# Kernel tuning notes

Measured on AMD Instinct MI355X. Metric: run time of the kernel, lower is better.

The kernel has to match this reference:

```python
import jax, jax.numpy as jnp
import numpy as np

B, D, K = 2048, 512, 32  # pairs, input_dim, feature_map_dim


def setup_inputs() -> dict:
    key = jax.random.key(0)
    k1, k2, kw, kv, ku = jax.random.split(key, 5)
    x1 = jax.random.normal(k1, (B, D), dtype=jnp.float32)
    x2 = jax.random.normal(k2, (B, D), dtype=jnp.float32)
    # glorot-style scaled params
    W = jax.random.normal(kw, (D, D, K), dtype=jnp.float32) * (1.0 / np.sqrt(D))
    V = jax.random.normal(kv, (K, 2 * D), dtype=jnp.float32) * (1.0 / np.sqrt(2 * D))
    U = jax.random.normal(ku, (K, 1), dtype=jnp.float32)
    b = jnp.zeros((K,), dtype=jnp.float32)
    return {"x1": x1, "x2": x2, "W": W, "V": V, "U": U, "b": b}


def reference(x1, x2, W, V, U, b):
    # Bilinear term: h[b,k] = x1[b]^T W[:,:,k] x2[b]
    h = jnp.einsum('bd,dek,be->bk', x1, W, x2)
    # Linear term: V[k] . concat(x1, x2)   (loop's V_out, batched)
    v_out = jnp.concatenate([x1, x2], axis=1) @ V.T  # [B, K]
    scores = jax.nn.relu(h + v_out + b)              # inneract
    # output per pair: sum_k U[k] * scores[k]
    return scores @ U[:, 0]  # [B]
```

## Files before the change

### kernel.cpp

```cpp
#include <hip/hip_runtime.h>
#include <hip/hip_bf16.h>


#define BATCH 2048
#define DIM 512
#define KF 32
#define NCOL (DIM * KF)
#define JT (NCOL / 128)

typedef __attribute__((ext_vector_type(8))) short bf16x8;
typedef __attribute__((ext_vector_type(4))) float f32x4;
typedef __attribute__((address_space(1))) const unsigned int gas_u32;
typedef __attribute__((address_space(3))) unsigned int las_u32;

static __device__ __forceinline__ ushort f2bf(float x) {
    __hip_bfloat16 h = __float2bfloat16(x);
    union { __hip_bfloat16 h; ushort u; } cv; cv.h = h;
    return cv.u;
}

__global__ void fused_prep_kernel(const float* __restrict__ x1,
                                  const float* __restrict__ x2,
                                  const float* __restrict__ W,
                                  const float* __restrict__ V,
                                  ushort* __restrict__ x1b,
                                  ushort* __restrict__ Wt,
                                  float* __restrict__ vout) {
    __shared__ __align__(16) char sbuf[32768];
    const int bx = blockIdx.x;
    const int t = threadIdx.x;

    if (bx < 256) {
        float (*xs)[1024] = (float(*)[1024])sbuf;
        const int b0 = bx * 8;
        #pragma unroll
        for (int it = 0; it < 4; ++it) {
            int q = it * 256 + t;
            int r = q >> 7;
            int c = (q & 127) * 4;
            *(float4*)&xs[r][c]       = *(const float4*)&x1[(size_t)(b0 + r) * DIM + c];
            *(float4*)&xs[r][512 + c] = *(const float4*)&x2[(size_t)(b0 + r) * DIM + c];
        }
        __syncthreads();
        const int lane = t & 63, w = t >> 6;
        #pragma unroll
        for (int rr = 0; rr < 2; ++rr) {
            const int r = w * 2 + rr;
            float4 xv[4];
            #pragma unroll
            for (int i = 0; i < 4; ++i)
                xv[i] = *(const float4*)&xs[r][i * 256 + lane * 4];
            #pragma unroll
            for (int k0 = 0; k0 < KF; k0 += 4) {
                float s[4] = {0.f, 0.f, 0.f, 0.f};
                #pragma unroll
                for (int kk = 0; kk < 4; ++kk) {
                    const float* vrow = V + (size_t)(k0 + kk) * 1024;
                    #pragma unroll
                    for (int i = 0; i < 4; ++i) {
                        float4 vv = *(const float4*)&vrow[i * 256 + lane * 4];
                        s[kk] += vv.x * xv[i].x + vv.y * xv[i].y + vv.z * xv[i].z + vv.w * xv[i].w;
                    }
                }
                #pragma unroll
                for (int kk = 0; kk < 4; ++kk) {
                    float v = s[kk];
                    #pragma unroll
                    for (int off = 32; off; off >>= 1) v += __shfl_down(v, off);
                    if (lane == 0) vout[(size_t)(b0 + r) * KF + k0 + kk] = v;
                }
            }
        }
    } else if (bx < 1280) {
        int i = (bx - 256) * 256 + t;
        float4 v = *((const float4*)x1 + i);
        ushort4 r;
        r.x = f2bf(v.x); r.y = f2bf(v.y); r.z = f2bf(v.z); r.w = f2bf(v.w);
        *((ushort4*)x1b + i) = r;
    } else {
        ushort (*lt)[65] = (ushort(*)[65])sbuf;
        const int bxl = bx - 1280;
        const int n0 = (bxl >> 3) * 64;
        const int d0 = (bxl & 7) * 64;
        #pragma unroll
        for (int it = 0; it < 4; ++it) {
            int q = it * 256 + t;
            int dl = q >> 4;
            int n4 = (q & 15) * 4;
            float4 v = *(const float4*)&W[(size_t)(d0 + dl) * NCOL + n0 + n4];
            lt[n4 + 0][dl] = f2bf(v.x);
            lt[n4 + 1][dl] = f2bf(v.y);
            lt[n4 + 2][dl] = f2bf(v.z);
            lt[n4 + 3][dl] = f2bf(v.w);
        }
        __syncthreads();
        #pragma unroll
        for (int it = 0; it < 4; ++it) {
            int q = it * 256 + t;
            int nl = q >> 4;
            int d4 = (q & 15) * 4;
            ushort4 o;
            o.x = lt[nl][d4 + 0]; o.y = lt[nl][d4 + 1];
            o.z = lt[nl][d4 + 2]; o.w = lt[nl][d4 + 3];
            *(ushort4*)&Wt[(size_t)(n0 + nl) * DIM + d0 + d4] = o;
        }
    }
}

__global__ void gemm_fused_kernel(const ushort* __restrict__ Ab,
                                  const ushort* __restrict__ Bt,
                                  const float* __restrict__ x2,
                                  float* __restrict__ hpart) {
    __shared__ __align__(16) char smem[16384];
    ushort* As = (ushort*)smem;
    ushort* Bs = (ushort*)(smem + 8192);
    float*  hp = (float*)smem;

    const int j = blockIdx.x;
    const int i = blockIdx.y;
    const int t = threadIdx.x;
    const int lane = t & 63, wid = t >> 6;
    const int wr = wid >> 1, wc = wid & 1;
    const int row0 = i * 128, col0 = j * 128;
    const int l15 = lane & 15, lk = (lane >> 4) * 8, lh = lane >> 4;

    const int sr = t >> 2;
    const int scsw = ((t & 3) ^ ((sr & 6) >> 1)) * 8;
    const int lksw = lk ^ ((l15 & 6) << 2);

    f32x4 acc[4][4] = {};

    for (int kt = 0; kt < DIM; kt += 32) {
        __builtin_amdgcn_global_load_lds(
            (gas_u32*)&Ab[(size_t)(row0 + sr) * DIM + kt + scsw],
            (las_u32*)&As[t * 8], 16, 0, 0);
        __builtin_amdgcn_global_load_lds(
            (gas_u32*)&Ab[(size_t)(row0 + 64 + sr) * DIM + kt + scsw],
            (las_u32*)&As[2048 + t * 8], 16, 0, 0);
        __builtin_amdgcn_global_load_lds(
            (gas_u32*)&Bt[(size_t)(col0 + sr) * DIM + kt + scsw],
            (las_u32*)&Bs[t * 8], 16, 0, 0);
        __builtin_amdgcn_global_load_lds(
            (gas_u32*)&Bt[(size_t)(col0 + 64 + sr) * DIM + kt + scsw],
            (las_u32*)&Bs[2048 + t * 8], 16, 0, 0);
        __syncthreads();
        bf16x8 af[4], bfr[4];
        #pragma unroll
        for (int m = 0; m < 4; ++m)
            af[m] = *(bf16x8*)&As[(wr * 64 + m * 16 + l15) * 32 + lksw];
        #pragma unroll
        for (int n = 0; n < 4; ++n)
            bfr[n] = *(bf16x8*)&Bs[(wc * 64 + n * 16 + l15) * 32 + lksw];
        #pragma unroll
        for (int m = 0; m < 4; ++m)
            #pragma unroll
            for (int n = 0; n < 4; ++n)
                acc[m][n] = __builtin_amdgcn_mfma_f32_16x16x32_bf16(af[m], bfr[n], acc[m][n], 0, 0, 0);
        __syncthreads();
    }

    const int e0 = j * 4 + wc * 2;
    if (wc == 0) {
        #pragma unroll
        for (int m = 0; m < 4; ++m) {
            #pragma unroll
            for (int reg = 0; reg < 4; ++reg) {
                int row = wr * 64 + m * 16 + lh * 4 + reg;
                float xa = x2[(size_t)(row0 + row) * DIM + e0];
                float xb = x2[(size_t)(row0 + row) * DIM + e0 + 1];
                hp[row * 32 + l15]      = acc[m][0][reg] * xa + acc[m][2][reg] * xb;
                hp[row * 32 + 16 + l15] = acc[m][1][reg] * xa + acc[m][3][reg] * xb;
            }
        }
    }
    __syncthreads();
    if (wc == 1) {
        #pragma unroll
        for (int m = 0; m < 4; ++m) {
            #pragma unroll
            for (int reg = 0; reg < 4; ++reg) {
                int row = wr * 64 + m * 16 + lh * 4 + reg;
                float xa = x2[(size_t)(row0 + row) * DIM + e0];
                float xb = x2[(size_t)(row0 + row) * DIM + e0 + 1];
                hp[row * 32 + l15]      += acc[m][0][reg] * xa + acc[m][2][reg] * xb;
                hp[row * 32 + 16 + l15] += acc[m][1][reg] * xa + acc[m][3][reg] * xb;
            }
        }
    }
    __syncthreads();
    #pragma unroll
    for (int q = 0; q < 4; ++q) {
        int idx = q * 1024 + t * 4;
        int row = idx >> 5, kf = idx & 31;
        *(float4*)&hpart[(size_t)(row0 + row) * (JT * KF) + j * KF + kf] = *(float4*)&hp[idx];
    }
}

__global__ void reduce_out_kernel(const float* __restrict__ hpart,
                                  const float* __restrict__ vout,
                                  const float* __restrict__ U,
                                  const float* __restrict__ bias,
                                  float* __restrict__ out) {
    const int b = blockIdx.x;
    const int t = threadIdx.x;
    __shared__ float4 hsm[256];
    __shared__ float hk[32];

    const float* hb = hpart + (size_t)b * (JT * KF);
    float4 a4 = {0.f, 0.f, 0.f, 0.f};
    #pragma unroll
    for (int p = 0; p < 4; ++p) {
        float4 v = *(const float4*)&hb[p * 1024 + t * 4];
        a4.x += v.x; a4.y += v.y; a4.z += v.z; a4.w += v.w;
    }
    hsm[t] = a4;
    __syncthreads();
    if (t < 8) {
        float4 s = {0.f, 0.f, 0.f, 0.f};
        #pragma unroll
        for (int g = 0; g < 32; ++g) {
            float4 v = hsm[g * 8 + t];
            s.x += v.x; s.y += v.y; s.z += v.z; s.w += v.w;
        }
        hk[t * 4 + 0] = s.x; hk[t * 4 + 1] = s.y;
        hk[t * 4 + 2] = s.z; hk[t * 4 + 3] = s.w;
    }
    __syncthreads();

    float val = 0.0f;
    if (t < 32) {
        float sc = hk[t] + vout[(size_t)b * KF + t] + bias[t];
        sc = fmaxf(sc, 0.0f);
        val = sc * U[t];
    }
    if (t < 64) {
        #pragma unroll
        for (int off = 16; off; off >>= 1) val += __shfl_down(val, off);
        if (t == 0) out[b] = val;
    }
}

extern "C" void kernel_launch(void* const* d_in, const int* in_sizes, int n_in,
                              void* d_out, int out_size, void* d_ws, size_t ws_size,
                              hipStream_t stream) {
    const float* x1   = (const float*)d_in[0];
    const float* x2   = (const float*)d_in[1];
    const float* W    = (const float*)d_in[2];
    const float* V    = (const float*)d_in[3];
    const float* U    = (const float*)d_in[4];
    const float* bias = (const float*)d_in[5];
    float* out = (float*)d_out;

    char* ws = (char*)d_ws;
    ushort* x1b = (ushort*)ws;
    ushort* Wt  = (ushort*)(ws + (size_t)2 * 1024 * 1024);
    float*  hp  = (float*)(ws + (size_t)18 * 1024 * 1024);
    float*  vo  = (float*)(ws + (size_t)50 * 1024 * 1024);

    fused_prep_kernel<<<dim3(3328), dim3(256), 0, stream>>>(x1, x2, W, V, x1b, Wt, vo);
    gemm_fused_kernel<<<dim3(JT, 16), dim3(256), 0, stream>>>(x1b, Wt, x2, hp);
    reduce_out_kernel<<<dim3(BATCH), dim3(256), 0, stream>>>(hp, vo, U, bias, out);
}
```

Before: 155.6 us.

## Accumulate four column tiles per GEMM block to shrink partial buffer and reduction

Each GEMM block now loops over four 128-column tiles and accumulates the x2-weighted partial h results in a dedicated LDS buffer, so the partial-sum buffer shrinks from 128 to 32 slices per row. The reduce kernel becomes one wavefront per batch row using xor shuffles instead of LDS and block barriers, and the grid shrinks by 4x. This cuts the partial-sum write and read traffic and the reduce launch overhead, but the GEMM grid drops from 2048 to 512 blocks and LDS use doubles, which may leave CUs underutilized.

```diff
diff --git a/kernel.cpp b/kernel.cpp
--- a/kernel.cpp
+++ b/kernel.cpp
@@ -7,6 +7,7 @@
 #define KF 32
 #define NCOL (DIM * KF)
 #define JT (NCOL / 128)
+#define JG 32
 
 typedef __attribute__((ext_vector_type(8))) short bf16x8;
 typedef __attribute__((ext_vector_type(4))) float f32x4;
@@ -111,88 +112,102 @@
                                   const ushort* __restrict__ Bt,
                                   const float* __restrict__ x2,
                                   float* __restrict__ hpart) {
-    __shared__ __align__(16) char smem[16384];
+    __shared__ __align__(16) char smem[32768];
     ushort* As = (ushort*)smem;
     ushort* Bs = (ushort*)(smem + 8192);
-    float*  hp = (float*)smem;
-
-    const int j = blockIdx.x;
+    float*  ha = (float*)(smem + 16384);
+
+    const int jg = blockIdx.x;
     const int i = blockIdx.y;
     const int t = threadIdx.x;
     const int lane = t & 63, wid = t >> 6;
     const int wr = wid >> 1, wc = wid & 1;
-    const int row0 = i * 128, col0 = j * 128;
+    const int row0 = i * 128;
     const int l15 = lane & 15, lk = (lane >> 4) * 8, lh = lane >> 4;
 
     const int sr = t >> 2;
     const int scsw = ((t & 3) ^ ((sr & 6) >> 1)) * 8;
     const int lksw = lk ^ ((l15 & 6) << 2);
 
-    f32x4 acc[4][4] = {};
-
-    for (int kt = 0; kt < DIM; kt += 32) {
-        __builtin_amdgcn_global_load_lds(
-            (gas_u32*)&Ab[(size_t)(row0 + sr) * DIM + kt + scsw],
-            (las_u32*)&As[t * 8], 16, 0, 0);
-        __builtin_amdgcn_global_load_lds(
-            (gas_u32*)&Ab[(size_t)(row0 + 64 + sr) * DIM + kt + scsw],
-            (las_u32*)&As[2048 + t * 8], 16, 0, 0);
-        __builtin_amdgcn_global_load_lds(
-            (gas_u32*)&Bt[(size_t)(col0 + sr) * DIM + kt + scsw],
-            (las_u32*)&Bs[t * 8], 16, 0, 0);
-        __builtin_amdgcn_global_load_lds(
-            (gas_u32*)&Bt[(size_t)(col0 + 64 + sr) * DIM + kt + scsw],
-            (las_u32*)&Bs[2048 + t * 8], 16, 0, 0);
-        __syncthreads();
-        bf16x8 af[4], bfr[4];
-        #pragma unroll
-        for (int m = 0; m < 4; ++m)
-            af[m] = *(bf16x8*)&As[(wr * 64 + m * 16 + l15) * 32 + lksw];
-        #pragma unroll
-        for (int n = 0; n < 4; ++n)
-            bfr[n] = *(bf16x8*)&Bs[(wc * 64 + n * 16 + l15) * 32 + lksw];
-        #pragma unroll
-        for (int m = 0; m < 4; ++m)
+    #pragma unroll
+    for (int it = 0; it < 4; ++it) {
+        float4 z = {0.f, 0.f, 0.f, 0.f};
+        *(float4*)&ha[(it * 256 + t) * 4] = z;
+    }
+    __syncthreads();
+
+    for (int jj = 0; jj < 4; ++jj) {
+        const int j = jg * 4 + jj;
+        const int col0 = j * 128;
+
+        f32x4 acc[4][4] = {};
+
+        for (int kt = 0; kt < DIM; kt += 32) {
+            __builtin_amdgcn_global_load_lds(
+                (gas_u32*)&Ab[(size_t)(row0 + sr) * DIM + kt + scsw],
+                (las_u32*)&As[t * 8], 16, 0, 0);
+            __builtin_amdgcn_global_load_lds(
+                (gas_u32*)&Ab[(size_t)(row0 + 64 + sr) * DIM + kt + scsw],
+                (las_u32*)&As[2048 + t * 8], 16, 0, 0);
+            __builtin_amdgcn_global_load_lds(
+                (gas_u32*)&Bt[(size_t)(col0 + sr) * DIM + kt + scsw],
+                (las_u32*)&Bs[t * 8], 16, 0, 0);
+            __builtin_amdgcn_global_load_lds(
+                (gas_u32*)&Bt[(size_t)(col0 + 64 + sr) * DIM + kt + scsw],
+                (las_u32*)&Bs[2048 + t * 8], 16, 0, 0);
+            __syncthreads();
+            bf16x8 af[4], bfr[4];
+            #pragma unroll
+            for (int m = 0; m < 4; ++m)
+                af[m] = *(bf16x8*)&As[(wr * 64 + m * 16 + l15) * 32 + lksw];
             #pragma unroll
             for (int n = 0; n < 4; ++n)
-                acc[m][n] = __builtin_amdgcn_mfma_f32_16x16x32_bf16(af[m], bfr[n], acc[m][n], 0, 0, 0);
-        __syncthreads();
-    }
-
-    const int e0 = j * 4 + wc * 2;
-    if (wc == 0) {
-        #pragma unroll
-        for (int m = 0; m < 4; ++m) {
-            #pragma unroll
-            for (int reg = 0; reg < 4; ++reg) {
-                int row = wr * 64 + m * 16 + lh * 4 + reg;
-                float xa = x2[(size_t)(row0 + row) * DIM + e0];
-                float xb = x2[(size_t)(row0 + row) * DIM + e0 + 1];
-                hp[row * 32 + l15]      = acc[m][0][reg] * xa + acc[m][2][reg] * xb;
-                hp[row * 32 + 16 + l15] = acc[m][1][reg] * xa + acc[m][3][reg] * xb;
+                bfr[n] = *(bf16x8*)&Bs[(wc * 64 + n * 16 + l15) * 32 + lksw];
+            #pragma unroll
+            for (int m = 0; m < 4; ++m)
+                #pragma unroll
+                for (int n = 0; n < 4; ++n)
+                    acc[m][n] = __builtin_amdgcn_mfma_f32_16x16x32_bf16(af[m], bfr[n], acc[m][n], 0, 0, 0);
+            __syncthreads();
+        }
+
+        const int e0 = j * 4 + wc * 2;
+        if (wc == 0) {
+            #pragma unroll
+            for (int m = 0; m < 4; ++m) {
+                #pragma unroll
+                for (int reg = 0; reg < 4; ++reg) {
+                    int row = wr * 64 + m * 16 + lh * 4 + reg;
+                    float xa = x2[(size_t)(row0 + row) * DIM + e0];
+                    float xb = x2[(size_t)(row0 + row) * DIM + e0 + 1];
+                    ha[row * 32 + l15]      += acc[m][0][reg] * xa + acc[m][2][reg] * xb;
+                    ha[row * 32 + 16 + l15] += acc[m][1][reg] * xa + acc[m][3][reg] * xb;
+                }
             }
         }
-    }
-    __syncthreads();
-    if (wc == 1) {
-        #pragma unroll
-        for (int m = 0; m < 4; ++m) {
-            #pragma unroll
-            for (int reg = 0; reg < 4; ++reg) {
-                int row = wr * 64 + m * 16 + lh * 4 + reg;
-                float xa = x2[(size_t)(row0 + row) * DIM + e0];
-                float xb = x2[(size_t)(row0 + row) * DIM + e0 + 1];
-                hp[row * 32 + l15]      += acc[m][0][reg] * xa + acc[m][2][reg] * xb;
-                hp[row * 32 + 16 + l15] += acc[m][1][reg] * xa + acc[m][3][reg] * xb;
+        __syncthreads();
+        if (wc == 1) {
+            #pragma unroll
+            for (int m = 0; m < 4; ++m) {
+                #pragma unroll
+                for (int reg = 0; reg < 4; ++reg) {
+                    int row = wr * 64 + m * 16 + lh * 4 + reg;
+                    float xa = x2[(size_t)(row0 + row) * DIM + e0];
+                    float xb = x2[(size_t)(row0 + row) * DIM + e0 + 1];
+                    ha[row * 32 + l15]      += acc[m][0][reg] * xa + acc[m][2][reg] * xb;
+                    ha[row * 32 + 16 + l15] += acc[m][1][reg] * xa + acc[m][3][reg] * xb;
+                }
             }
         }
-    }
-    __syncthreads();
+        __syncthreads();
+    }
+
     #pragma unroll
     for (int q = 0; q < 4; ++q) {
         int idx = q * 1024 + t * 4;
         int row = idx >> 5, kf = idx & 31;
-        *(float4*)&hpart[(size_t)(row0 + row) * (JT * KF) + j * KF + kf] = *(float4*)&hp[idx];
+        *(float4*)&hpart[(size_t)(row0 + row) * (JG * KF) + jg * KF + kf] =
+            *(float4*)&ha[idx];
     }
 }
 
@@ -201,43 +216,37 @@
                                   const float* __restrict__ U,
                                   const float* __restrict__ bias,
                                   float* __restrict__ out) {
-    const int b = blockIdx.x;
     const int t = threadIdx.x;
-    __shared__ float4 hsm[256];
-    __shared__ float hk[32];
-
-    const float* hb = hpart + (size_t)b * (JT * KF);
+    const int lane = t & 63, w = t >> 6;
+    const int b = blockIdx.x * 4 + w;
+
+    const float* hb = hpart + (size_t)b * (JG * KF);
+    const int jr = lane >> 3;
+    const int kq = lane & 7;
     float4 a4 = {0.f, 0.f, 0.f, 0.f};
     #pragma unroll
     for (int p = 0; p < 4; ++p) {
-        float4 v = *(const float4*)&hb[p * 1024 + t * 4];
+        float4 v = *(const float4*)&hb[(p * 8 + jr) * KF + kq * 4];
         a4.x += v.x; a4.y += v.y; a4.z += v.z; a4.w += v.w;
     }
-    hsm[t] = a4;
-    __syncthreads();
-    if (t < 8) {
-        float4 s = {0.f, 0.f, 0.f, 0.f};
-        #pragma unroll
-        for (int g = 0; g < 32; ++g) {
-            float4 v = hsm[g * 8 + t];
-            s.x += v.x; s.y += v.y; s.z += v.z; s.w += v.w;
-        }
-        hk[t * 4 + 0] = s.x; hk[t * 4 + 1] = s.y;
-        hk[t * 4 + 2] = s.z; hk[t * 4 + 3] = s.w;
-    }
-    __syncthreads();
-
-    float val = 0.0f;
-    if (t < 32) {
-        float sc = hk[t] + vout[(size_t)b * KF + t] + bias[t];
-        sc = fmaxf(sc, 0.0f);
-        val = sc * U[t];
-    }
-    if (t < 64) {
-        #pragma unroll
-        for (int off = 16; off; off >>= 1) val += __shfl_down(val, off);
-        if (t == 0) out[b] = val;
-    }
+    #pragma unroll
+    for (int mask = 8; mask <= 32; mask <<= 1) {
+        a4.x += __shfl_xor(a4.x, mask);
+        a4.y += __shfl_xor(a4.y, mask);
+        a4.z += __shfl_xor(a4.z, mask);
+        a4.w += __shfl_xor(a4.w, mask);
+    }
+    float4 vo4 = *(const float4*)&vout[(size_t)b * KF + kq * 4];
+    float4 bi4 = *(const float4*)&bias[kq * 4];
+    float4 u4  = *(const float4*)&U[kq * 4];
+    float p0 = fmaxf(a4.x + vo4.x + bi4.x, 0.f) * u4.x;
+    float p1 = fmaxf(a4.y + vo4.y + bi4.y, 0.f) * u4.y;
+    float p2 = fmaxf(a4.z + vo4.z + bi4.z, 0.f) * u4.z;
+    float p3 = fmaxf(a4.w + vo4.w + bi4.w, 0.f) * u4.w;
+    float p = p0 + p1 + p2 + p3;
+    #pragma unroll
+    for (int mask = 1; mask <= 4; mask <<= 1) p += __shfl_xor(p, mask);
+    if (lane == 0) out[b] = p;
 }
 
 extern "C" void kernel_launch(void* const* d_in, const int* in_sizes, int n_in,
@@ -254,10 +263,10 @@
     char* ws = (char*)d_ws;
     ushort* x1b = (ushort*)ws;
     ushort* Wt  = (ushort*)(ws + (size_t)2 * 1024 * 1024);
-    float*  hp  = (float*)(ws + (size_t)18 * 1024 * 1024);
-    float*  vo  = (float*)(ws + (size_t)50 * 1024 * 1024);
+    float*  hp  = (float*)(ws + (size_t)19 * 1024 * 1024);
+    float*  vo  = (float*)(ws + (size_t)27 * 1024 * 1024);
 
     fused_prep_kernel<<<dim3(3328), dim3(256), 0, stream>>>(x1, x2, W, V, x1b, Wt, vo);
-    gemm_fused_kernel<<<dim3(JT, 16), dim3(256), 0, stream>>>(x1b, Wt, x2, hp);
-    reduce_out_kernel<<<dim3(BATCH), dim3(256), 0, stream>>>(hp, vo, U, bias, out);
-}
+    gemm_fused_kernel<<<dim3(JG, 16), dim3(256), 0, stream>>>(x1b, Wt, x2, hp);
+    reduce_out_kernel<<<dim3(BATCH / 4), dim3(256), 0, stream>>>(hp, vo, U, bias, out);
+}
```

Result: slower. 280.4 us (+80.2%).
